# Kernel tuning notes

Hardware: AMD Instinct MI355X
Metric: run time of the kernel (lower is better)

Reference implementation:

```python
import jax, jax.numpy as jnp
import numpy as np

HIDDEN = 2048
NUM_HEADS = 32
NUM_KV_HEADS = 8
HEAD_DIM = HIDDEN // NUM_HEADS  # 64


def setup_inputs() -> dict:
    key = jax.random.key(0)
    ks = jax.random.split(key, 5)
    s = 0.02
    x = jax.random.normal(ks[0], (2, 2048, HIDDEN), dtype=jnp.float32)
    Wq = jax.random.normal(ks[1], (HIDDEN, NUM_HEADS * HEAD_DIM), dtype=jnp.float32) * s
    Wk = jax.random.normal(ks[2], (HIDDEN, NUM_KV_HEADS * HEAD_DIM), dtype=jnp.float32) * s
    Wv = jax.random.normal(ks[3], (HIDDEN, NUM_KV_HEADS * HEAD_DIM), dtype=jnp.float32) * s
    Wo = jax.random.normal(ks[4], (NUM_HEADS * HEAD_DIM, HIDDEN), dtype=jnp.float32) * s
    return {"x": x, "Wq": Wq, "Wk": Wk, "Wv": Wv, "Wo": Wo}


def reference(x, Wq, Wk, Wv, Wo):
    b, s, _ = x.shape
    # projections: [b, s, h, d] -> [b, h, s, d]
    q = (x @ Wq).reshape(b, s, NUM_HEADS, HEAD_DIM).transpose(0, 2, 1, 3)
    k = (x @ Wk).reshape(b, s, NUM_KV_HEADS, HEAD_DIM).transpose(0, 2, 1, 3)
    v = (x @ Wv).reshape(b, s, NUM_KV_HEADS, HEAD_DIM).transpose(0, 2, 1, 3)
    rep = NUM_HEADS // NUM_KV_HEADS
    # repeat_interleave along head dim (consecutive copies), matching torch
    k = jnp.repeat(k, rep, axis=1)
    v = jnp.repeat(v, rep, axis=1)
    scale = HEAD_DIM ** (-0.5)
    attn = jnp.einsum("bhqd,bhkd->bhqk", q, k) * scale  # [b,h,s,s]
    attn = jax.nn.softmax(attn, axis=-1)
    out = jnp.einsum("bhqk,bhkd->bhqd", attn, v)
    out = out.transpose(0, 2, 1, 3).reshape(b, s, NUM_HEADS * HEAD_DIM)
    return out @ Wo
```

## Files before the change

kernel.cpp:

```cpp
#include <hip/hip_runtime.h>

typedef __attribute__((ext_vector_type(8))) short short8;
typedef __attribute__((ext_vector_type(4))) float f32x4;
typedef __attribute__((ext_vector_type(4))) unsigned short u16x4;
typedef __attribute__((ext_vector_type(8))) unsigned short u16x8;

__device__ __forceinline__ unsigned short f2bf(float f) {
  union { float f; unsigned u; } v; v.f = f;
  unsigned r = v.u + 0x7FFFu + ((v.u >> 16) & 1u);
  return (unsigned short)(r >> 16);
}

#define GLL16(g, l) \
  __builtin_amdgcn_global_load_lds((const __attribute__((address_space(1))) void*)(g), \
                                   (__attribute__((address_space(3))) void*)(l), 16, 0, 0)

__device__ __forceinline__ void tpose_body(const float* __restrict__ in,
                                           unsigned short* __restrict__ out,
                                           int C, int ldo, int c0, int r0,
                                           float (*tile)[33], int tx, int ty) {
#pragma unroll
  for (int i = 0; i < 4; ++i)
    tile[ty + i * 8][tx] = in[(size_t)(r0 + ty + i * 8) * C + c0 + tx];
  __syncthreads();
#pragma unroll
  for (int i = 0; i < 4; ++i)
    out[(size_t)(c0 + ty + i * 8) * ldo + r0 + tx] = f2bf(tile[tx][ty + i * 8]);
}

__global__ __launch_bounds__(256) void prep_kernel(const float* __restrict__ x,
                                                   const float* __restrict__ Wq,
                                                   const float* __restrict__ Wk,
                                                   const float* __restrict__ Wv,
                                                   const float* __restrict__ Wo,
                                                   unsigned short* __restrict__ xb,
                                                   unsigned short* __restrict__ wqkvt,
                                                   unsigned short* __restrict__ wot) {
  __shared__ float tile[32][33];
  const int bid = blockIdx.x;
  if (bid < 4096) {
    const int i = bid * 256 + threadIdx.x;
    const f32x4* p = (const f32x4*)x;
    f32x4 a = p[2 * i], b = p[2 * i + 1];
    u16x8 r;
    r[0] = f2bf(a[0]); r[1] = f2bf(a[1]); r[2] = f2bf(a[2]); r[3] = f2bf(a[3]);
    r[4] = f2bf(b[0]); r[5] = f2bf(b[1]); r[6] = f2bf(b[2]); r[7] = f2bf(b[3]);
    ((u16x8*)xb)[i] = r;
    return;
  }
  const int tx = threadIdx.x & 31, ty = threadIdx.x >> 5;
  int b2 = bid - 4096;
  if (b2 < 4096) {
    tpose_body(Wq, wqkvt, 2048, 2048, (b2 & 63) * 32, (b2 >> 6) * 32, tile, tx, ty);
    return;
  }
  b2 -= 4096;
  if (b2 < 1024) {
    tpose_body(Wk, wqkvt + (size_t)2048 * 2048, 512, 2048, (b2 & 15) * 32, (b2 >> 4) * 32, tile, tx, ty);
    return;
  }
  b2 -= 1024;
  if (b2 < 1024) {
    tpose_body(Wv, wqkvt + (size_t)2560 * 2048, 512, 2048, (b2 & 15) * 32, (b2 >> 4) * 32, tile, tx, ty);
    return;
  }
  b2 -= 1024;
  tpose_body(Wo, wot, 2048, 2048, (b2 & 63) * 32, (b2 >> 6) * 32, tile, tx, ty);
}

__global__ __launch_bounds__(512) void gemm_qkv_kernel(const unsigned short* __restrict__ A,
                                                       const unsigned short* __restrict__ BT,
                                                       unsigned short* __restrict__ Cq,
                                                       unsigned short* __restrict__ VT) {
  __shared__ unsigned short As[2][128 * 32];
  __shared__ unsigned short Bs[2][128 * 32];
  const int tid = threadIdx.x;
  const int wave = tid >> 6, lane = tid & 63;
  const int r16 = lane & 15, g = lane >> 4;
  const int n0 = blockIdx.x * 128, m0 = blockIdx.y * 128;
  const int wr = wave >> 2, wc = wave & 3;
  f32x4 acc[4][2] = {};
  const int so = tid * 16;
  const int srow = so >> 6, ske = (so & 63) >> 1;

  auto STAGE = [&](int kt, int bufi) {
    const int k0 = kt * 32;
    GLL16(A + (size_t)(m0 + srow) * 2048 + k0 + ske, (char*)As[bufi] + wave * 1024);
    GLL16(BT + (size_t)(n0 + srow) * 2048 + k0 + ske, (char*)Bs[bufi] + wave * 1024);
  };
  STAGE(0, 0);
  __syncthreads();
  for (int kt = 0; kt < 64; ++kt) {
    const int cur = kt & 1;
    if (kt < 63) STAGE(kt + 1, cur ^ 1);
    short8 af[4], bfr[2];
#pragma unroll
    for (int mi = 0; mi < 4; ++mi) {
      const int row = wr * 64 + mi * 16 + r16;
      af[mi] = *(const short8*)((const char*)As[cur] + row * 64 + g * 16);
    }
#pragma unroll
    for (int ni = 0; ni < 2; ++ni) {
      const int row = wc * 32 + ni * 16 + r16;
      bfr[ni] = *(const short8*)((const char*)Bs[cur] + row * 64 + g * 16);
    }
#pragma unroll
    for (int mi = 0; mi < 4; ++mi)
#pragma unroll
      for (int ni = 0; ni < 2; ++ni)
        acc[mi][ni] = __builtin_amdgcn_mfma_f32_16x16x32_bf16(af[mi], bfr[ni], acc[mi][ni], 0, 0, 0);
    __syncthreads();
  }
  const float qs = 0.18033688f;
#pragma unroll
  for (int mi = 0; mi < 4; ++mi) {
#pragma unroll
    for (int ni = 0; ni < 2; ++ni) {
      const int n = n0 + wc * 32 + ni * 16 + r16;
      const int mb = m0 + wr * 64 + mi * 16 + g * 4;
      f32x4 v = acc[mi][ni];
      if (n < 2560) {
        const float s = (n < 2048) ? qs : 1.0f;
#pragma unroll
        for (int r = 0; r < 4; ++r) Cq[(size_t)(mb + r) * 3072 + n] = f2bf(v[r] * s);
      } else {
        const int d = n - 2560;
        const int bb = mb >> 11, s0 = mb & 2047;
        const int s0p = (s0 & ~31) | (((s0 >> 2) & 3) << 3) | (((s0 >> 4) & 1) << 2);
        u16x4 pk;
#pragma unroll
        for (int r = 0; r < 4; ++r) pk[r] = f2bf(v[r]);
        *(u16x4*)(VT + (size_t)(bb * 512 + d) * 2048 + s0p) = pk;
      }
    }
  }
}

__global__ __launch_bounds__(512) void gemm_out_kernel(const unsigned short* __restrict__ A,
                                                       const unsigned short* __restrict__ BT,
                                                       float* __restrict__ Co) {
  __shared__ unsigned short As[2][128 * 32];
  __shared__ unsigned short Bs[2][128 * 32];
  const int tid = threadIdx.x;
  const int wave = tid >> 6, lane = tid & 63;
  const int r16 = lane & 15, g = lane >> 4;
  const int n0 = blockIdx.x * 128, m0 = blockIdx.y * 128;
  const int wr = wave >> 2, wc = wave & 3;
  f32x4 acc[4][2] = {};
  const int so = tid * 16;
  const int srow = so >> 6, ske = (so & 63) >> 1;

  auto STAGE = [&](int kt, int bufi) {
    const int k0 = kt * 32;
    GLL16(A + (size_t)(m0 + srow) * 2048 + k0 + ske, (char*)As[bufi] + wave * 1024);
    GLL16(BT + (size_t)(n0 + srow) * 2048 + k0 + ske, (char*)Bs[bufi] + wave * 1024);
  };
  STAGE(0, 0);
  __syncthreads();
  for (int kt = 0; kt < 64; ++kt) {
    const int cur = kt & 1;
    if (kt < 63) STAGE(kt + 1, cur ^ 1);
    short8 af[4], bfr[2];
#pragma unroll
    for (int mi = 0; mi < 4; ++mi) {
      const int row = wr * 64 + mi * 16 + r16;
      af[mi] = *(const short8*)((const char*)As[cur] + row * 64 + g * 16);
    }
#pragma unroll
    for (int ni = 0; ni < 2; ++ni) {
      const int row = wc * 32 + ni * 16 + r16;
      bfr[ni] = *(const short8*)((const char*)Bs[cur] + row * 64 + g * 16);
    }
#pragma unroll
    for (int mi = 0; mi < 4; ++mi)
#pragma unroll
      for (int ni = 0; ni < 2; ++ni)
        acc[mi][ni] = __builtin_amdgcn_mfma_f32_16x16x32_bf16(af[mi], bfr[ni], acc[mi][ni], 0, 0, 0);
    __syncthreads();
  }
#pragma unroll
  for (int mi = 0; mi < 4; ++mi)
#pragma unroll
    for (int ni = 0; ni < 2; ++ni) {
      const int n = n0 + wc * 32 + ni * 16 + r16;
      const int mb = m0 + wr * 64 + mi * 16 + g * 4;
      f32x4 v = acc[mi][ni];
#pragma unroll
      for (int r = 0; r < 4; ++r) Co[(size_t)(mb + r) * 2048 + n] = v[r];
    }
}

__global__ __launch_bounds__(512) void attn_kernel(const unsigned short* __restrict__ QKV,
                                                   const unsigned short* __restrict__ VT,
                                                   unsigned short* __restrict__ O) {
  __shared__ unsigned short Ks[4][64 * 64];
  __shared__ unsigned short Vs[4][64 * 64];
  const int tid = threadIdx.x;
  const int wave = tid >> 6, lane = tid & 63;
  const int r16 = lane & 15, g = lane >> 4;
  const int qt = blockIdx.x, bh = blockIdx.y;
  const int b = bh >> 5, h = bh & 31, kvh = h >> 2;
  const int qtok0 = b * 2048 + qt * 128 + wave * 16;
  short8 qf[2];
#pragma unroll
  for (int kh = 0; kh < 2; ++kh)
    qf[kh] = *(const short8*)(QKV + (size_t)(qtok0 + r16) * 3072 + h * 64 + kh * 32 + g * 8);
  union { unsigned u[4]; short8 s; } ones;
  ones.u[0] = ones.u[1] = ones.u[2] = ones.u[3] = 0x3F803F80u;
  f32x4 oa[4] = {};
  f32x4 lacc = {};
  const int swz = (r16 & 7) << 4;
  const int b0 = r16 * 128 + ((g * 16) ^ swz);
  const int b1 = r16 * 128 + ((64 + g * 16) ^ swz);
  const unsigned short* Kb = QKV + (size_t)b * 2048 * 3072 + 2048 + kvh * 64;
  const unsigned short* Vb = VT + (size_t)(b * 512 + kvh * 64) * 2048;
  const int so = wave * 1024 + lane * 16;

  auto STAGE = [&](int t, int bufi) {
    const int kv0 = t * 64;
    const int row = so >> 7;
    const int c = ((((so >> 4) & 7) ^ (row & 7))) * 8;
    GLL16(Kb + (size_t)(kv0 + row) * 3072 + c, (char*)Ks[bufi] + wave * 1024);
    GLL16(Vb + (size_t)row * 2048 + kv0 + c, (char*)Vs[bufi] + wave * 1024);
  };
  auto COMPUTE = [&](int buf) {
    f32x4 sc[4];
    __builtin_amdgcn_s_setprio(1);
#pragma unroll
    for (int jt = 0; jt < 4; ++jt) {
      short8 kf0 = *(const short8*)((const char*)Ks[buf] + jt * 2048 + b0);
      short8 kf1 = *(const short8*)((const char*)Ks[buf] + jt * 2048 + b1);
      f32x4 z = {-8.f, -8.f, -8.f, -8.f};
      z = __builtin_amdgcn_mfma_f32_16x16x32_bf16(kf0, qf[0], z, 0, 0, 0);
      z = __builtin_amdgcn_mfma_f32_16x16x32_bf16(kf1, qf[1], z, 0, 0, 0);
      sc[jt] = z;
    }
    __builtin_amdgcn_s_setprio(0);
    short8 pa[2];
    {
      unsigned pk[4][2];
#pragma unroll
      for (int jt = 0; jt < 4; ++jt) {
        float p0 = __builtin_amdgcn_exp2f(sc[jt][0]);
        float p1 = __builtin_amdgcn_exp2f(sc[jt][1]);
        float p2 = __builtin_amdgcn_exp2f(sc[jt][2]);
        float p3 = __builtin_amdgcn_exp2f(sc[jt][3]);
        asm("v_cvt_pk_bf16_f32 %0, %1, %2" : "=v"(pk[jt][0]) : "v"(p0), "v"(p1));
        asm("v_cvt_pk_bf16_f32 %0, %1, %2" : "=v"(pk[jt][1]) : "v"(p2), "v"(p3));
      }
#pragma unroll
      for (int kh = 0; kh < 2; ++kh) {
        union { unsigned u[4]; short8 s; } pu;
        pu.u[0] = pk[2 * kh][0]; pu.u[1] = pk[2 * kh][1];
        pu.u[2] = pk[2 * kh + 1][0]; pu.u[3] = pk[2 * kh + 1][1];
        pa[kh] = pu.s;
      }
    }
    __builtin_amdgcn_s_setprio(1);
    lacc = __builtin_amdgcn_mfma_f32_16x16x32_bf16(pa[0], ones.s, lacc, 0, 0, 0);
    lacc = __builtin_amdgcn_mfma_f32_16x16x32_bf16(pa[1], ones.s, lacc, 0, 0, 0);
#pragma unroll
    for (int dt = 0; dt < 4; ++dt) {
      short8 vf0 = *(const short8*)((const char*)Vs[buf] + dt * 2048 + b0);
      short8 vf1 = *(const short8*)((const char*)Vs[buf] + dt * 2048 + b1);
      oa[dt] = __builtin_amdgcn_mfma_f32_16x16x32_bf16(pa[0], vf0, oa[dt], 0, 0, 0);
      oa[dt] = __builtin_amdgcn_mfma_f32_16x16x32_bf16(pa[1], vf1, oa[dt], 0, 0, 0);
    }
    __builtin_amdgcn_s_setprio(0);
  };

  STAGE(0, 0);
  STAGE(1, 1);
  __syncthreads();
  for (int j = 0; j < 16; ++j) {
    const int cur = (j & 1) << 1;
    if (j < 15) {
      STAGE(2 * j + 2, cur ^ 2);
      STAGE(2 * j + 3, (cur ^ 2) + 1);
    }
    COMPUTE(cur);
    COMPUTE(cur + 1);
    __syncthreads();
  }
#pragma unroll
  for (int dt = 0; dt < 4; ++dt)
#pragma unroll
    for (int r = 0; r < 4; ++r)
      O[(size_t)(qtok0 + g * 4 + r) * 2048 + h * 64 + dt * 16 + r16] =
          f2bf(oa[dt][r] / lacc[r]);
}

extern "C" void kernel_launch(void* const* d_in, const int* in_sizes, int n_in,
                              void* d_out, int out_size, void* d_ws, size_t ws_size,
                              hipStream_t stream) {
  const float* x  = (const float*)d_in[0];
  const float* Wq = (const float*)d_in[1];
  const float* Wk = (const float*)d_in[2];
  const float* Wv = (const float*)d_in[3];
  const float* Wo = (const float*)d_in[4];
  char* w = (char*)d_ws;
  unsigned short* xb    = (unsigned short*)(w);
  unsigned short* wqkvt = (unsigned short*)(w + 16777216);
  unsigned short* wot   = (unsigned short*)(w + 29360128);
  unsigned short* qkv   = (unsigned short*)(w + 37748736);
  unsigned short* vt    = (unsigned short*)(w + 62914560);
  unsigned short* ob    = (unsigned short*)(w + 67108864);
  float* out = (float*)d_out;

  prep_kernel<<<14336, 256, 0, stream>>>(x, Wq, Wk, Wv, Wo, xb, wqkvt, wot);
  gemm_qkv_kernel<<<dim3(24, 32), 512, 0, stream>>>(xb, wqkvt, qkv, vt);
  attn_kernel<<<dim3(16, 64), 512, 0, stream>>>(qkv, vt, ob);
  gemm_out_kernel<<<dim3(16, 32), 512, 0, stream>>>(ob, wot, out);
}
```

Before: 216.6 us.

## Deepen GEMM global-to-LDS pipeline to four stages with explicit vmcnt waits

Both projection GEMMs move from double-buffered LDS staging with a full __syncthreads per k-step to a four-buffer ring that keeps three tiles of global_load_lds in flight. Each step waits on vmcnt for the oldest tile, issues one raw s_barrier, then prefetches and computes. The goal is to hide global memory latency and drop the extra barrier per iteration. In exchange, LDS per block doubles to 64 KB, which may cut occupancy, and correctness now depends on the hand-set vmcnt counts.

```diff
diff --git a/kernel.cpp b/kernel.cpp
--- a/kernel.cpp
+++ b/kernel.cpp
@@ -72,8 +72,8 @@
                                                        const unsigned short* __restrict__ BT,
                                                        unsigned short* __restrict__ Cq,
                                                        unsigned short* __restrict__ VT) {
-  __shared__ unsigned short As[2][128 * 32];
-  __shared__ unsigned short Bs[2][128 * 32];
+  __shared__ unsigned short As[4][128 * 32];
+  __shared__ unsigned short Bs[4][128 * 32];
   const int tid = threadIdx.x;
   const int wave = tid >> 6, lane = tid & 63;
   const int r16 = lane & 15, g = lane >> 4;
@@ -88,29 +88,44 @@
     GLL16(A + (size_t)(m0 + srow) * 2048 + k0 + ske, (char*)As[bufi] + wave * 1024);
     GLL16(BT + (size_t)(n0 + srow) * 2048 + k0 + ske, (char*)Bs[bufi] + wave * 1024);
   };
-  STAGE(0, 0);
-  __syncthreads();
-  for (int kt = 0; kt < 64; ++kt) {
-    const int cur = kt & 1;
-    if (kt < 63) STAGE(kt + 1, cur ^ 1);
+  auto COMPUTE = [&](int bufi) {
     short8 af[4], bfr[2];
 #pragma unroll
     for (int mi = 0; mi < 4; ++mi) {
       const int row = wr * 64 + mi * 16 + r16;
-      af[mi] = *(const short8*)((const char*)As[cur] + row * 64 + g * 16);
+      af[mi] = *(const short8*)((const char*)As[bufi] + row * 64 + g * 16);
     }
 #pragma unroll
     for (int ni = 0; ni < 2; ++ni) {
       const int row = wc * 32 + ni * 16 + r16;
-      bfr[ni] = *(const short8*)((const char*)Bs[cur] + row * 64 + g * 16);
+      bfr[ni] = *(const short8*)((const char*)Bs[bufi] + row * 64 + g * 16);
     }
 #pragma unroll
     for (int mi = 0; mi < 4; ++mi)
 #pragma unroll
       for (int ni = 0; ni < 2; ++ni)
         acc[mi][ni] = __builtin_amdgcn_mfma_f32_16x16x32_bf16(af[mi], bfr[ni], acc[mi][ni], 0, 0, 0);
-    __syncthreads();
-  }
+  };
+
+  STAGE(0, 0);
+  STAGE(1, 1);
+  STAGE(2, 2);
+  for (int kt = 0; kt < 61; ++kt) {
+    asm volatile("s_waitcnt vmcnt(4)" ::: "memory");
+    __builtin_amdgcn_s_barrier();
+    STAGE(kt + 3, (kt + 3) & 3);
+    COMPUTE(kt & 3);
+  }
+  asm volatile("s_waitcnt vmcnt(4)" ::: "memory");
+  __builtin_amdgcn_s_barrier();
+  COMPUTE(1);
+  asm volatile("s_waitcnt vmcnt(2)" ::: "memory");
+  __builtin_amdgcn_s_barrier();
+  COMPUTE(2);
+  asm volatile("s_waitcnt vmcnt(0)" ::: "memory");
+  __builtin_amdgcn_s_barrier();
+  COMPUTE(3);
+
   const float qs = 0.18033688f;
 #pragma unroll
   for (int mi = 0; mi < 4; ++mi) {
@@ -139,8 +154,8 @@
 __global__ __launch_bounds__(512) void gemm_out_kernel(const unsigned short* __restrict__ A,
                                                        const unsigned short* __restrict__ BT,
                                                        float* __restrict__ Co) {
-  __shared__ unsigned short As[2][128 * 32];
-  __shared__ unsigned short Bs[2][128 * 32];
+  __shared__ unsigned short As[4][128 * 32];
+  __shared__ unsigned short Bs[4][128 * 32];
   const int tid = threadIdx.x;
   const int wave = tid >> 6, lane = tid & 63;
   const int r16 = lane & 15, g = lane >> 4;
@@ -155,29 +170,44 @@
     GLL16(A + (size_t)(m0 + srow) * 2048 + k0 + ske, (char*)As[bufi] + wave * 1024);
     GLL16(BT + (size_t)(n0 + srow) * 2048 + k0 + ske, (char*)Bs[bufi] + wave * 1024);
   };
-  STAGE(0, 0);
-  __syncthreads();
-  for (int kt = 0; kt < 64; ++kt) {
-    const int cur = kt & 1;
-    if (kt < 63) STAGE(kt + 1, cur ^ 1);
+  auto COMPUTE = [&](int bufi) {
     short8 af[4], bfr[2];
 #pragma unroll
     for (int mi = 0; mi < 4; ++mi) {
       const int row = wr * 64 + mi * 16 + r16;
-      af[mi] = *(const short8*)((const char*)As[cur] + row * 64 + g * 16);
+      af[mi] = *(const short8*)((const char*)As[bufi] + row * 64 + g * 16);
     }
 #pragma unroll
     for (int ni = 0; ni < 2; ++ni) {
       const int row = wc * 32 + ni * 16 + r16;
-      bfr[ni] = *(const short8*)((const char*)Bs[cur] + row * 64 + g * 16);
+      bfr[ni] = *(const short8*)((const char*)Bs[bufi] + row * 64 + g * 16);
     }
 #pragma unroll
     for (int mi = 0; mi < 4; ++mi)
 #pragma unroll
       for (int ni = 0; ni < 2; ++ni)
         acc[mi][ni] = __builtin_amdgcn_mfma_f32_16x16x32_bf16(af[mi], bfr[ni], acc[mi][ni], 0, 0, 0);
-    __syncthreads();
-  }
+  };
+
+  STAGE(0, 0);
+  STAGE(1, 1);
+  STAGE(2, 2);
+  for (int kt = 0; kt < 61; ++kt) {
+    asm volatile("s_waitcnt vmcnt(4)" ::: "memory");
+    __builtin_amdgcn_s_barrier();
+    STAGE(kt + 3, (kt + 3) & 3);
+    COMPUTE(kt & 3);
+  }
+  asm volatile("s_waitcnt vmcnt(4)" ::: "memory");
+  __builtin_amdgcn_s_barrier();
+  COMPUTE(1);
+  asm volatile("s_waitcnt vmcnt(2)" ::: "memory");
+  __builtin_amdgcn_s_barrier();
+  COMPUTE(2);
+  asm volatile("s_waitcnt vmcnt(0)" ::: "memory");
+  __builtin_amdgcn_s_barrier();
+  COMPUTE(3);
+
 #pragma unroll
   for (int mi = 0; mi < 4; ++mi)
 #pragma unroll
```

New measurement: 228.2 us. +5.4%, slower.
